# Kernel optimization log

Hardware: AMD Instinct MI355X
Metric: run time of the kernel (lower is better)

## Reference

```python
import jax, jax.numpy as jnp
import numpy as np

N, E = 50000, 1600000
IN_DIM, EMBED, OUT = 512, 128, 64


def setup_inputs() -> dict:
    key = jax.random.key(0)
    k = jax.random.split(key, 8)
    x = jax.random.normal(k[0], (N, IN_DIM), dtype=jnp.float32)
    edge_index = jax.random.randint(k[1], (2, E), 0, N, dtype=jnp.int32)
    W_dense = jax.random.normal(k[2], (EMBED, IN_DIM), dtype=jnp.float32) * 0.02
    b_dense = jnp.zeros((EMBED,), dtype=jnp.float32)
    W_gat = jax.random.normal(k[3], (OUT, EMBED), dtype=jnp.float32) * 0.05
    att_src = jax.random.normal(k[4], (OUT,), dtype=jnp.float32) * 0.1
    att_dst = jax.random.normal(k[5], (OUT,), dtype=jnp.float32) * 0.1
    b_gat = jnp.zeros((OUT,), dtype=jnp.float32)
    return {"x": x, "edge_index": edge_index, "W_dense": W_dense, "b_dense": b_dense,
            "W_gat": W_gat, "att_src": att_src, "att_dst": att_dst, "b_gat": b_gat}


def reference(x, edge_index, W_dense, b_dense, W_gat, att_src, att_dst, b_gat):
    # dense -> LeakyReLU(0.01) (nn.LeakyReLU default)
    h = jax.nn.leaky_relu(x @ W_dense.T + b_dense, negative_slope=0.01)  # [N, EMBED]
    n = h.shape[0]
    # GATConv (PyG, heads=1, add_self_loops=True, negative_slope=0.2)
    loops = jnp.arange(n, dtype=edge_index.dtype)
    src = jnp.concatenate([edge_index[0], loops])
    dst = jnp.concatenate([edge_index[1], loops])
    g = h @ W_gat.T  # [N, OUT]
    a_src = g @ att_src  # [N]
    a_dst = g @ att_dst  # [N]
    e = jax.nn.leaky_relu(a_src[src] + a_dst[dst], negative_slope=0.2)  # [E+N]
    # segment softmax over destination neighborhoods (self loops guarantee non-empty)
    m = jax.ops.segment_max(e, dst, num_segments=n)
    e = jnp.exp(e - m[dst])
    denom = jax.ops.segment_sum(e, dst, num_segments=n)
    alpha = e / denom[dst]
    out = jax.ops.segment_sum(g[src] * alpha[:, None], dst, num_segments=n) + b_gat
    # original returns ([embed_x], [embed_x]); we return the single embedding tensor
    return out
```

## Files before the change

### kernel.cpp

```cpp
#include <hip/hip_runtime.h>
#include <math.h>

#define IN_DIM 512
#define EMBED 128
#define OUT_DIM 64
#define NBPAD 256
#define SEGSH 12
#define CAP_LDS 10240

typedef __attribute__((ext_vector_type(8))) short bf16x8;
typedef __attribute__((ext_vector_type(4))) float f32x4;

__device__ __forceinline__ float lrelu(float v, float s) { return v > 0.f ? v : v * s; }

__device__ __forceinline__ float readlane_f(float v, int l) {
  return __int_as_float(__builtin_amdgcn_readlane(__float_as_int(v), l));
}

__device__ __forceinline__ unsigned short f2bf(float f) {
  unsigned int u = __float_as_uint(f);
  u += 0x7fff + ((u >> 16) & 1);
  return (unsigned short)(u >> 16);
}
__device__ __forceinline__ float bf2f(unsigned short h) {
  return __uint_as_float(((unsigned int)h) << 16);
}

__device__ __forceinline__ unsigned int cvt_pk_bf16(float a, float b) {
  unsigned int r;
  asm("v_cvt_pk_bf16_f32 %0, %1, %2" : "=v"(r) : "v"(a), "v"(b));
  return r;
}

__device__ __forceinline__ void gl_lds16(const void* g, void* l) {
  __builtin_amdgcn_global_load_lds(
      (const __attribute__((address_space(1))) unsigned int*)g,
      (__attribute__((address_space(3))) unsigned int*)l, 16, 0, 0);
}

#define LDA 40

__global__ __launch_bounds__(256) void split_w_kernel(
    const float* __restrict__ W, unsigned short* __restrict__ Wh,
    unsigned short* __restrict__ Wl, int total) {
  int i = (blockIdx.x * 256 + threadIdx.x) * 4;
  if (i >= total) return;
  float4 v = *(const float4*)(W + i);
  unsigned int h0 = cvt_pk_bf16(v.x, v.y);
  unsigned int h1 = cvt_pk_bf16(v.z, v.w);
  float r0 = v.x - __uint_as_float(h0 << 16);
  float r1 = v.y - __uint_as_float(h0 & 0xffff0000u);
  float r2 = v.z - __uint_as_float(h1 << 16);
  float r3 = v.w - __uint_as_float(h1 & 0xffff0000u);
  unsigned int l0 = cvt_pk_bf16(r0, r1);
  unsigned int l1 = cvt_pk_bf16(r2, r3);
  uint2 hh = make_uint2(h0, h1);
  uint2 ll = make_uint2(l0, l1);
  *(uint2*)(Wh + i) = hh;
  *(uint2*)(Wl + i) = ll;
}

__global__ __launch_bounds__(256) void gemm1_mfma_kernel(
    const float* __restrict__ x, const unsigned short* __restrict__ Wdh,
    const unsigned short* __restrict__ Wdl, const float* __restrict__ bd,
    float* __restrict__ h, int N) {
  __shared__ __align__(16) unsigned char Afp[16384];
  __shared__ __align__(16) unsigned char Bhs[8192];
  __shared__ __align__(16) unsigned char Bls[8192];

  const int tid = threadIdx.x;
  const int lane = tid & 63;
  const int wid = tid >> 6;
  const int mblk = blockIdx.x * 128;
  const int quad = lane >> 4;
  const int l15 = lane & 15;

  const char* asrc[4];
  void* adst[4];
#pragma unroll
  for (int i = 0; i < 4; ++i) {
    int chunk = i * 256 + tid;
    int row = chunk >> 3, ch = chunk & 7;
    int rg = mblk + row;
    if (rg >= N) rg = N - 1;
    asrc[i] = (const char*)x + (size_t)rg * (IN_DIM * 4) + ((ch ^ (row & 7)) << 4);
    adst[i] = Afp + chunk * 16;
  }
  const char* bsrcH[2];
  const char* bsrcL[2];
  void* bdstH[2];
  void* bdstL[2];
#pragma unroll
  for (int i = 0; i < 2; ++i) {
    int chunk = i * 256 + tid;
    int row = chunk >> 2, ch = chunk & 3;
    int cs = ch ^ ((row >> 1) & 3);
    size_t srcoff = (size_t)row * (IN_DIM * 2) + (cs << 4);
    bsrcH[i] = (const char*)Wdh + srcoff;
    bsrcL[i] = (const char*)Wdl + srcoff;
    bdstH[i] = Bhs + chunk * 16;
    bdstL[i] = Bls + chunk * 16;
  }

  f32x4 acc[2][8];
#pragma unroll
  for (int i = 0; i < 2; ++i)
#pragma unroll
    for (int j = 0; j < 8; ++j) acc[i][j] = (f32x4){0.f, 0.f, 0.f, 0.f};

  int aoff[2][2];
#pragma unroll
  for (int mi = 0; mi < 2; ++mi) {
    int row = wid * 32 + mi * 16 + l15;
    int sw = (row & 7) << 4;
#pragma unroll
    for (int hf = 0; hf < 2; ++hf)
      aoff[mi][hf] = row * 128 + (((quad << 5) | (hf << 4)) ^ sw);
  }
  int boff[8];
#pragma unroll
  for (int ni = 0; ni < 8; ++ni) {
    int row = ni * 16 + l15;
    boff[ni] = row * 64 + ((quad ^ ((row >> 1) & 3)) << 4);
  }

  for (int k0 = 0; k0 < IN_DIM; k0 += 32) {
    __syncthreads();
    const size_t ka = (size_t)k0 * 4;
    const size_t kb = (size_t)k0 * 2;
#pragma unroll
    for (int i = 0; i < 4; ++i) gl_lds16(asrc[i] + ka, adst[i]);
#pragma unroll
    for (int i = 0; i < 2; ++i) {
      gl_lds16(bsrcH[i] + kb, bdstH[i]);
      gl_lds16(bsrcL[i] + kb, bdstL[i]);
    }
    __syncthreads();

    bf16x8 AH[2], AL[2];
#pragma unroll
    for (int mi = 0; mi < 2; ++mi) {
      float4 f0 = *(const float4*)(Afp + aoff[mi][0]);
      float4 f1 = *(const float4*)(Afp + aoff[mi][1]);
      float av[8] = {f0.x, f0.y, f0.z, f0.w, f1.x, f1.y, f1.z, f1.w};
      union { unsigned int u[4]; bf16x8 v; } H, L;
#pragma unroll
      for (int i = 0; i < 4; ++i) {
        unsigned int hp = cvt_pk_bf16(av[2 * i], av[2 * i + 1]);
        float q0 = av[2 * i] - __uint_as_float(hp << 16);
        float q1 = av[2 * i + 1] - __uint_as_float(hp & 0xffff0000u);
        H.u[i] = hp;
        L.u[i] = cvt_pk_bf16(q0, q1);
      }
      AH[mi] = H.v;
      AL[mi] = L.v;
    }

#pragma unroll
    for (int hf = 0; hf < 2; ++hf) {
      bf16x8 BH[4], BL[4];
#pragma unroll
      for (int j = 0; j < 4; ++j) {
        BH[j] = *(const bf16x8*)(Bhs + boff[hf * 4 + j]);
        BL[j] = *(const bf16x8*)(Bls + boff[hf * 4 + j]);
      }
#pragma unroll
      for (int mi = 0; mi < 2; ++mi)
#pragma unroll
        for (int j = 0; j < 4; ++j) {
          int ni = hf * 4 + j;
          acc[mi][ni] = __builtin_amdgcn_mfma_f32_16x16x32_bf16(AH[mi], BH[j], acc[mi][ni], 0, 0, 0);
          acc[mi][ni] = __builtin_amdgcn_mfma_f32_16x16x32_bf16(AL[mi], BH[j], acc[mi][ni], 0, 0, 0);
          acc[mi][ni] = __builtin_amdgcn_mfma_f32_16x16x32_bf16(AH[mi], BL[j], acc[mi][ni], 0, 0, 0);
        }
    }
  }

#pragma unroll
  for (int mi = 0; mi < 2; ++mi)
#pragma unroll
    for (int ni = 0; ni < 8; ++ni) {
      int n = ni * 16 + l15;
      float b = bd[n];
#pragma unroll
      for (int r = 0; r < 4; ++r) {
        int m = mblk + wid * 32 + mi * 16 + quad * 4 + r;
        if (m < N) h[(size_t)m * EMBED + n] = lrelu(acc[mi][ni][r] + b, 0.01f);
      }
    }
}

__global__ __launch_bounds__(256) void gemm2_mfma_kernel(
    const float* __restrict__ h, const float* __restrict__ Wg,
    const float* __restrict__ att_src, const float* __restrict__ att_dst,
    float* __restrict__ g, float* __restrict__ a_src, float* __restrict__ a_dst,
    int N) {
  __shared__ __align__(16) unsigned short Ah[128][LDA];
  __shared__ __align__(16) unsigned short Al[128][LDA];
  __shared__ __align__(16) unsigned short Bh[64][LDA];
  __shared__ __align__(16) unsigned short Bl[64][LDA];

  const int tid = threadIdx.x;
  const int lane = tid & 63;
  const int wid = tid >> 6;
  const int wr = wid >> 1, wc = wid & 1;
  const int mblk = blockIdx.x * 128;
  const int quad = lane >> 4;
  const int l15 = lane & 15;

  const int arow = tid >> 1, acb = (tid & 1) * 16;
  const int brow = tid >> 2, bcb = (tid & 3) * 8;
  const bool avalid = (mblk + arow) < N;
  const float* aptr = h + (size_t)(mblk + arow) * EMBED + acb;
  const float* bptr = Wg + (size_t)brow * EMBED + bcb;

  f32x4 acc[4][2];
#pragma unroll
  for (int i = 0; i < 4; ++i)
#pragma unroll
    for (int j = 0; j < 2; ++j) acc[i][j] = (f32x4){0.f, 0.f, 0.f, 0.f};

  float4 t0, t1, t2, t3, u0, u1;
  auto do_load = [&](int k0) {
    if (avalid) {
      t0 = *(const float4*)(aptr + k0);
      t1 = *(const float4*)(aptr + k0 + 4);
      t2 = *(const float4*)(aptr + k0 + 8);
      t3 = *(const float4*)(aptr + k0 + 12);
    } else {
      t0 = t1 = t2 = t3 = make_float4(0.f, 0.f, 0.f, 0.f);
    }
    u0 = *(const float4*)(bptr + k0);
    u1 = *(const float4*)(bptr + k0 + 4);
  };
  do_load(0);

  for (int k0 = 0; k0 < EMBED; k0 += 32) {
    float av[16] = {t0.x, t0.y, t0.z, t0.w, t1.x, t1.y, t1.z, t1.w,
                    t2.x, t2.y, t2.z, t2.w, t3.x, t3.y, t3.z, t3.w};
    union { unsigned short us[16]; uint4 v[2]; } AH, AL;
#pragma unroll
    for (int i = 0; i < 16; ++i) {
      unsigned short hi = f2bf(av[i]);
      AH.us[i] = hi;
      AL.us[i] = f2bf(av[i] - bf2f(hi));
    }
    float bv[8] = {u0.x, u0.y, u0.z, u0.w, u1.x, u1.y, u1.z, u1.w};
    union { unsigned short us[8]; uint4 v; } BH, BL;
#pragma unroll
    for (int i = 0; i < 8; ++i) {
      unsigned short hi = f2bf(bv[i]);
      BH.us[i] = hi;
      BL.us[i] = f2bf(bv[i] - bf2f(hi));
    }

    __syncthreads();
    *(uint4*)&Ah[arow][acb] = AH.v[0];
    *(uint4*)&Ah[arow][acb + 8] = AH.v[1];
    *(uint4*)&Al[arow][acb] = AL.v[0];
    *(uint4*)&Al[arow][acb + 8] = AL.v[1];
    *(uint4*)&Bh[brow][bcb] = BH.v;
    *(uint4*)&Bl[brow][bcb] = BL.v;
    __syncthreads();

    if (k0 + 32 < EMBED) do_load(k0 + 32);

    bf16x8 ah[4], al[4], bh[2], bl[2];
#pragma unroll
    for (int mi = 0; mi < 4; ++mi) {
      int r = wr * 64 + mi * 16 + l15;
      ah[mi] = *(const bf16x8*)&Ah[r][quad * 8];
      al[mi] = *(const bf16x8*)&Al[r][quad * 8];
    }
#pragma unroll
    for (int ni = 0; ni < 2; ++ni) {
      int r = wc * 32 + ni * 16 + l15;
      bh[ni] = *(const bf16x8*)&Bh[r][quad * 8];
      bl[ni] = *(const bf16x8*)&Bl[r][quad * 8];
    }
#pragma unroll
    for (int mi = 0; mi < 4; ++mi)
#pragma unroll
      for (int ni = 0; ni < 2; ++ni) {
        acc[mi][ni] = __builtin_amdgcn_mfma_f32_16x16x32_bf16(ah[mi], bh[ni], acc[mi][ni], 0, 0, 0);
        acc[mi][ni] = __builtin_amdgcn_mfma_f32_16x16x32_bf16(al[mi], bh[ni], acc[mi][ni], 0, 0, 0);
        acc[mi][ni] = __builtin_amdgcn_mfma_f32_16x16x32_bf16(ah[mi], bl[ni], acc[mi][ni], 0, 0, 0);
      }
  }

  float as_[2], ad_[2];
#pragma unroll
  for (int ni = 0; ni < 2; ++ni) {
    int n = wc * 32 + ni * 16 + l15;
    as_[ni] = att_src[n];
    ad_[ni] = att_dst[n];
  }
#pragma unroll
  for (int mi = 0; mi < 4; ++mi) {
#pragma unroll
    for (int r = 0; r < 4; ++r) {
      int m = mblk + wr * 64 + mi * 16 + quad * 4 + r;
      float ps = acc[mi][0][r] * as_[0] + acc[mi][1][r] * as_[1];
      float pd = acc[mi][0][r] * ad_[0] + acc[mi][1][r] * ad_[1];
#pragma unroll
      for (int d = 1; d < 16; d <<= 1) {
        ps += __shfl_xor(ps, d, 64);
        pd += __shfl_xor(pd, d, 64);
      }
      if (m < N) {
#pragma unroll
        for (int ni = 0; ni < 2; ++ni) {
          int n = wc * 32 + ni * 16 + l15;
          g[(size_t)m * OUT_DIM + n] = acc[mi][ni][r];
        }
        if (l15 == 0 && wc == 0) {
          a_src[m] = ps;
          a_dst[m] = pd;
        }
      }
    }
  }
  __syncthreads();
#pragma unroll
  for (int mi = 0; mi < 4; ++mi) {
#pragma unroll
    for (int r = 0; r < 4; ++r) {
      int m = mblk + wr * 64 + mi * 16 + quad * 4 + r;
      float ps = acc[mi][0][r] * as_[0] + acc[mi][1][r] * as_[1];
      float pd = acc[mi][0][r] * ad_[0] + acc[mi][1][r] * ad_[1];
#pragma unroll
      for (int d = 1; d < 16; d <<= 1) {
        ps += __shfl_xor(ps, d, 64);
        pd += __shfl_xor(pd, d, 64);
      }
      if (m < N && l15 == 0 && wc == 1) {
        atomicAdd(&a_src[m], ps);
        atomicAdd(&a_dst[m], pd);
      }
    }
  }
}

__global__ __launch_bounds__(256) void hist_count_kernel(
    const int* __restrict__ ei, int* __restrict__ histT, int nblkP, int E,
    int N) {
  __shared__ int cnt[NBPAD];
  const int t = threadIdx.x;
  cnt[t] = 0;
  __syncthreads();
  const int T = E + N;
  const int base = blockIdx.x << SEGSH;
#pragma unroll
  for (int q = 0; q < (1 << SEGSH) / 256; ++q) {
    int i = base + q * 256 + t;
    if (i < T) {
      int d = (i < E) ? ei[E + i] : (i - E);
      atomicAdd(&cnt[d >> 8], 1);
    }
  }
  __syncthreads();
  histT[(size_t)t * nblkP + blockIdx.x] = cnt[t];
}

__global__ __launch_bounds__(256) void row_scan_kernel(
    int* __restrict__ histT, int* __restrict__ bucket_tot, int nblkP) {
  __shared__ int sc[256];
  const int t = threadIdx.x;
  int* row = histT + (size_t)blockIdx.x * nblkP;
  const int per = (nblkP + 255) / 256;
  int loc[8];
  int sum = 0;
#pragma unroll 4
  for (int j = 0; j < per; ++j) {
    int idx = t * per + j;
    int v = (idx < nblkP) ? row[idx] : 0;
    loc[j] = sum;
    sum += v;
  }
  sc[t] = sum;
  __syncthreads();
  for (int dlt = 1; dlt < 256; dlt <<= 1) {
    int add = (t >= dlt) ? sc[t - dlt] : 0;
    __syncthreads();
    sc[t] += add;
    __syncthreads();
  }
  const int off = sc[t] - sum;
#pragma unroll 4
  for (int j = 0; j < per; ++j) {
    int idx = t * per + j;
    if (idx < nblkP) row[idx] = off + loc[j];
  }
  if (t == 255) bucket_tot[blockIdx.x] = sc[255];
}

__global__ __launch_bounds__(256) void base_scan_kernel(
    const int* __restrict__ bucket_tot, int* __restrict__ bucket_base,
    int* __restrict__ offsets, int N, int T) {
  __shared__ int sc[256];
  const int t = threadIdx.x;
  int v = bucket_tot[t];
  sc[t] = v;
  __syncthreads();
  for (int dlt = 1; dlt < 256; dlt <<= 1) {
    int add = (t >= dlt) ? sc[t - dlt] : 0;
    __syncthreads();
    sc[t] += add;
    __syncthreads();
  }
  bucket_base[t] = sc[t] - v;
  if (t == 0) offsets[N] = T;
}

__global__ __launch_bounds__(256) void bin_kernel(
    const int* __restrict__ ei, const int* __restrict__ histT,
    const int* __restrict__ bucket_base, int* __restrict__ stageB, int nblkP,
    int E, int N) {
  __shared__ int cnt[NBPAD];
  __shared__ int basev[NBPAD];
  const int t = threadIdx.x;
  cnt[t] = 0;
  basev[t] = bucket_base[t] + histT[(size_t)t * nblkP + blockIdx.x];
  __syncthreads();
  const int T = E + N;
  const int base = blockIdx.x << SEGSH;
#pragma unroll
  for (int q = 0; q < (1 << SEGSH) / 256; ++q) {
    int i = base + q * 256 + t;
    if (i < T) {
      int s, d;
      if (i < E) {
        s = ei[i];
        d = ei[E + i];
      } else {
        s = d = i - E;
      }
      int b = d >> 8;
      int r = atomicAdd(&cnt[b], 1);
      stageB[basev[b] + r] = (s << 8) | (d & 255);
    }
  }
}

__global__ __launch_bounds__(256) void build_kernel(
    const int* __restrict__ stageB, const int* __restrict__ bucket_base,
    const int* __restrict__ bucket_tot, const float* __restrict__ a_src,
    const float* __restrict__ a_dst, int* __restrict__ offsets,
    int2* __restrict__ csr_pack, int N) {
  __shared__ int cnt[256];
  __shared__ int pre[256];
  __shared__ int cur[256];
  __shared__ int2 buf[CAP_LDS];
  const int b = blockIdx.x;
  const int t = threadIdx.x;
  const int base = bucket_base[b];
  const int tot = bucket_tot[b];
  cnt[t] = 0;
  __syncthreads();
  const int* sp = stageB + base;
  for (int i = t; i < tot; i += 256) atomicAdd(&cnt[sp[i] & 255], 1);
  __syncthreads();
  int v = cnt[t];
  pre[t] = v;
  __syncthreads();
  for (int dlt = 1; dlt < 256; dlt <<= 1) {
    int add = (t >= dlt) ? pre[t - dlt] : 0;
    __syncthreads();
    pre[t] += add;
    __syncthreads();
  }
  const int excl = pre[t] - v;
  cur[t] = excl;
  const int d_self = (b << 8) | t;
  if (d_self < N) offsets[d_self] = base + excl;
  __syncthreads();
  for (int i = t; i < tot; i += 256) {
    int rec = sp[i];
    int dl = rec & 255;
    int s = rec >> 8;
    float e = a_src[s] + a_dst[(b << 8) | dl];
    e = e > 0.f ? e : 0.2f * e;
    int pos = atomicAdd(&cur[dl], 1);
    int2 r2 = make_int2(s, __float_as_int(e));
    if (pos < CAP_LDS)
      buf[pos] = r2;
    else
      csr_pack[base + pos] = r2;
  }
  __syncthreads();
  const int lim = min(tot, CAP_LDS);
  for (int i = t; i < lim; i += 256) csr_pack[base + i] = buf[i];
}

__global__ __launch_bounds__(256) void aggregate_kernel(
    const int* __restrict__ offsets, const int2* __restrict__ csr_pack,
    const float* __restrict__ g, const float* __restrict__ b_gat,
    float* __restrict__ out, int N) {
  const int lane = threadIdx.x & 63;
  const int node = blockIdx.x * 4 + (threadIdx.x >> 6);
  if (node >= N) return;
  const int beg = offsets[node], end = offsets[node + 1];

  float m = -1e30f;
  for (int j = beg + lane; j < end; j += 64)
    m = fmaxf(m, __int_as_float(csr_pack[j].y));
#pragma unroll
  for (int d = 1; d < 64; d <<= 1) m = fmaxf(m, __shfl_xor(m, d, 64));

  float l = 0.f;
  for (int j = beg + lane; j < end; j += 64)
    l += __expf(__int_as_float(csr_pack[j].y) - m);
#pragma unroll
  for (int d = 1; d < 64; d <<= 1) l += __shfl_xor(l, d, 64);
  const float inv_l = 1.f / l;

  float acc0 = 0.f, acc1 = 0.f, acc2 = 0.f, acc3 = 0.f;
  for (int jb = beg; jb < end; jb += 64) {
    int j = jb + lane;
    float p = 0.f;
    int s = 0;
    if (j < end) {
      int2 rec = csr_pack[j];
      p = __expf(__int_as_float(rec.y) - m) * inv_l;
      s = rec.x;
    }
    const int cnt = min(64, end - jb);
    int jj = 0;
    for (; jj + 4 <= cnt; jj += 4) {
      int s0 = __builtin_amdgcn_readlane(s, jj);
      int s1 = __builtin_amdgcn_readlane(s, jj + 1);
      int s2 = __builtin_amdgcn_readlane(s, jj + 2);
      int s3 = __builtin_amdgcn_readlane(s, jj + 3);
      float p0 = readlane_f(p, jj);
      float p1 = readlane_f(p, jj + 1);
      float p2 = readlane_f(p, jj + 2);
      float p3 = readlane_f(p, jj + 3);
      acc0 += p0 * g[((size_t)s0 << 6) + lane];
      acc1 += p1 * g[((size_t)s1 << 6) + lane];
      acc2 += p2 * g[((size_t)s2 << 6) + lane];
      acc3 += p3 * g[((size_t)s3 << 6) + lane];
    }
    for (; jj < cnt; ++jj) {
      int s0 = __builtin_amdgcn_readlane(s, jj);
      float p0 = readlane_f(p, jj);
      acc0 += p0 * g[((size_t)s0 << 6) + lane];
    }
  }
  out[(size_t)node * OUT_DIM + lane] = (acc0 + acc1) + (acc2 + acc3) + b_gat[lane];
}

extern "C" void kernel_launch(void* const* d_in, const int* in_sizes, int n_in,
                              void* d_out, int out_size, void* d_ws, size_t ws_size,
                              hipStream_t stream) {
  const float* x = (const float*)d_in[0];
  const int* ei = (const int*)d_in[1];
  const float* Wd = (const float*)d_in[2];
  const float* bd = (const float*)d_in[3];
  const float* Wg = (const float*)d_in[4];
  const float* att_src = (const float*)d_in[5];
  const float* att_dst = (const float*)d_in[6];
  const float* bg = (const float*)d_in[7];
  float* out = (float*)d_out;

  const int N = in_sizes[0] / IN_DIM;
  const int E = in_sizes[1] / 2;
  const int T = E + N;
  const int NB = (N + 255) >> 8;
  const int nblkP = (T + (1 << SEGSH) - 1) >> SEGSH;

  char* ws = (char*)d_ws;
  size_t off = 0;
  auto alloc = [&](size_t bytes) -> void* {
    void* p = ws + off;
    off += (bytes + 15) & ~(size_t)15;
    return p;
  };
  float* h = (float*)alloc((size_t)N * EMBED * 4);
  float* g = (float*)alloc((size_t)N * OUT_DIM * 4);
  float* a_src = (float*)alloc((size_t)N * 4);
  float* a_dst = (float*)alloc((size_t)N * 4);
  int* offsets = (int*)alloc((size_t)(N + 1) * 4);
  int* histT = (int*)alloc((size_t)NBPAD * nblkP * 4);
  int* bucket_base = (int*)alloc((size_t)NBPAD * 4);
  int* bucket_tot = (int*)alloc((size_t)NBPAD * 4);
  int* stageB = (int*)alloc((size_t)T * 4);
  int2* csr_pack = (int2*)alloc((size_t)T * 8);
  unsigned short* Wdh = (unsigned short*)alloc((size_t)EMBED * IN_DIM * 2);
  unsigned short* Wdl = (unsigned short*)alloc((size_t)EMBED * IN_DIM * 2);

  const int WTOT = EMBED * IN_DIM;
  hipLaunchKernelGGL(split_w_kernel, dim3(WTOT / 1024), dim3(256), 0, stream,
                     Wd, Wdh, Wdl, WTOT);
  hipLaunchKernelGGL(gemm1_mfma_kernel, dim3((N + 127) / 128), dim3(256), 0,
                     stream, x, Wdh, Wdl, bd, h, N);
  hipLaunchKernelGGL(gemm2_mfma_kernel, dim3((N + 127) / 128), dim3(256), 0,
                     stream, h, Wg, att_src, att_dst, g, a_src, a_dst, N);
  hipLaunchKernelGGL(hist_count_kernel, dim3(nblkP), dim3(256), 0, stream,
                     ei, histT, nblkP, E, N);
  hipLaunchKernelGGL(row_scan_kernel, dim3(NBPAD), dim3(256), 0, stream,
                     histT, bucket_tot, nblkP);
  hipLaunchKernelGGL(base_scan_kernel, dim3(1), dim3(256), 0, stream,
                     bucket_tot, bucket_base, offsets, N, T);
  hipLaunchKernelGGL(bin_kernel, dim3(nblkP), dim3(256), 0, stream,
                     ei, histT, bucket_base, stageB, nblkP, E, N);
  hipLaunchKernelGGL(build_kernel, dim3(NB), dim3(256), 0, stream,
                     stageB, bucket_base, bucket_tot, a_src, a_dst, offsets,
                     csr_pack, N);
  hipLaunchKernelGGL(aggregate_kernel, dim3((N + 3) / 4), dim3(256), 0, stream,
                     offsets, csr_pack, g, bg, out, N);
}
```

Baseline: 315.9 us.

## Halve gemm1 row tile and process two nodes per wavefront in aggregation

The first GEMM now uses 64-row tiles instead of 128, which doubles the grid and cuts per-block LDS and accumulator registers to raise occupancy over the 50k-row problem. The aggregation kernel now splits each wavefront into two 32-lane halves, each handling one destination node and loading float2 feature pairs via shuffles instead of readlane. With about 33 edges per node on average, this avoids leaving half the lanes idle on the softmax and gather loops. The cost is less B-tile reuse in the GEMM and divergence when the two nodes in a wave have different degrees.

```diff
diff --git a/kernel.cpp b/kernel.cpp
--- a/kernel.cpp
+++ b/kernel.cpp
@@ -64,21 +64,21 @@
     const float* __restrict__ x, const unsigned short* __restrict__ Wdh,
     const unsigned short* __restrict__ Wdl, const float* __restrict__ bd,
     float* __restrict__ h, int N) {
-  __shared__ __align__(16) unsigned char Afp[16384];
+  __shared__ __align__(16) unsigned char Afp[8192];
   __shared__ __align__(16) unsigned char Bhs[8192];
   __shared__ __align__(16) unsigned char Bls[8192];
 
   const int tid = threadIdx.x;
   const int lane = tid & 63;
   const int wid = tid >> 6;
-  const int mblk = blockIdx.x * 128;
+  const int mblk = blockIdx.x * 64;
   const int quad = lane >> 4;
   const int l15 = lane & 15;
 
-  const char* asrc[4];
-  void* adst[4];
-#pragma unroll
-  for (int i = 0; i < 4; ++i) {
+  const char* asrc[2];
+  void* adst[2];
+#pragma unroll
+  for (int i = 0; i < 2; ++i) {
     int chunk = i * 256 + tid;
     int row = chunk >> 3, ch = chunk & 7;
     int rg = mblk + row;
@@ -102,20 +102,17 @@
     bdstL[i] = Bls + chunk * 16;
   }
 
-  f32x4 acc[2][8];
-#pragma unroll
-  for (int i = 0; i < 2; ++i)
-#pragma unroll
-    for (int j = 0; j < 8; ++j) acc[i][j] = (f32x4){0.f, 0.f, 0.f, 0.f};
-
-  int aoff[2][2];
-#pragma unroll
-  for (int mi = 0; mi < 2; ++mi) {
-    int row = wid * 32 + mi * 16 + l15;
+  f32x4 acc[8];
+#pragma unroll
+  for (int j = 0; j < 8; ++j) acc[j] = (f32x4){0.f, 0.f, 0.f, 0.f};
+
+  int aoff[2];
+  {
+    int row = wid * 16 + l15;
     int sw = (row & 7) << 4;
 #pragma unroll
     for (int hf = 0; hf < 2; ++hf)
-      aoff[mi][hf] = row * 128 + (((quad << 5) | (hf << 4)) ^ sw);
+      aoff[hf] = row * 128 + (((quad << 5) | (hf << 4)) ^ sw);
   }
   int boff[8];
 #pragma unroll
@@ -129,7 +126,7 @@
     const size_t ka = (size_t)k0 * 4;
     const size_t kb = (size_t)k0 * 2;
 #pragma unroll
-    for (int i = 0; i < 4; ++i) gl_lds16(asrc[i] + ka, adst[i]);
+    for (int i = 0; i < 2; ++i) gl_lds16(asrc[i] + ka, adst[i]);
 #pragma unroll
     for (int i = 0; i < 2; ++i) {
       gl_lds16(bsrcH[i] + kb, bdstH[i]);
@@ -137,11 +134,10 @@
     }
     __syncthreads();
 
-    bf16x8 AH[2], AL[2];
-#pragma unroll
-    for (int mi = 0; mi < 2; ++mi) {
-      float4 f0 = *(const float4*)(Afp + aoff[mi][0]);
-      float4 f1 = *(const float4*)(Afp + aoff[mi][1]);
+    bf16x8 AH, AL;
+    {
+      float4 f0 = *(const float4*)(Afp + aoff[0]);
+      float4 f1 = *(const float4*)(Afp + aoff[1]);
       float av[8] = {f0.x, f0.y, f0.z, f0.w, f1.x, f1.y, f1.z, f1.w};
       union { unsigned int u[4]; bf16x8 v; } H, L;
 #pragma unroll
@@ -152,8 +148,8 @@
         H.u[i] = hp;
         L.u[i] = cvt_pk_bf16(q0, q1);
       }
-      AH[mi] = H.v;
-      AL[mi] = L.v;
+      AH = H.v;
+      AL = L.v;
     }
 
 #pragma unroll
@@ -165,29 +161,25 @@
         BL[j] = *(const bf16x8*)(Bls + boff[hf * 4 + j]);
       }
 #pragma unroll
-      for (int mi = 0; mi < 2; ++mi)
-#pragma unroll
-        for (int j = 0; j < 4; ++j) {
-          int ni = hf * 4 + j;
-          acc[mi][ni] = __builtin_amdgcn_mfma_f32_16x16x32_bf16(AH[mi], BH[j], acc[mi][ni], 0, 0, 0);
-          acc[mi][ni] = __builtin_amdgcn_mfma_f32_16x16x32_bf16(AL[mi], BH[j], acc[mi][ni], 0, 0, 0);
-          acc[mi][ni] = __builtin_amdgcn_mfma_f32_16x16x32_bf16(AH[mi], BL[j], acc[mi][ni], 0, 0, 0);
-        }
-    }
-  }
-
-#pragma unroll
-  for (int mi = 0; mi < 2; ++mi)
-#pragma unroll
-    for (int ni = 0; ni < 8; ++ni) {
-      int n = ni * 16 + l15;
-      float b = bd[n];
-#pragma unroll
-      for (int r = 0; r < 4; ++r) {
-        int m = mblk + wid * 32 + mi * 16 + quad * 4 + r;
-        if (m < N) h[(size_t)m * EMBED + n] = lrelu(acc[mi][ni][r] + b, 0.01f);
-      }
-    }
+      for (int j = 0; j < 4; ++j) {
+        int ni = hf * 4 + j;
+        acc[ni] = __builtin_amdgcn_mfma_f32_16x16x32_bf16(AH, BH[j], acc[ni], 0, 0, 0);
+        acc[ni] = __builtin_amdgcn_mfma_f32_16x16x32_bf16(AL, BH[j], acc[ni], 0, 0, 0);
+        acc[ni] = __builtin_amdgcn_mfma_f32_16x16x32_bf16(AH, BL[j], acc[ni], 0, 0, 0);
+      }
+    }
+  }
+
+#pragma unroll
+  for (int ni = 0; ni < 8; ++ni) {
+    int n = ni * 16 + l15;
+    float b = bd[n];
+#pragma unroll
+    for (int r = 0; r < 4; ++r) {
+      int m = mblk + wid * 16 + quad * 4 + r;
+      if (m < N) h[(size_t)m * EMBED + n] = lrelu(acc[ni][r] + b, 0.01f);
+    }
+  }
 }
 
 __global__ __launch_bounds__(256) void gemm2_mfma_kernel(
@@ -497,26 +489,34 @@
     const float* __restrict__ g, const float* __restrict__ b_gat,
     float* __restrict__ out, int N) {
   const int lane = threadIdx.x & 63;
-  const int node = blockIdx.x * 4 + (threadIdx.x >> 6);
-  if (node >= N) return;
-  const int beg = offsets[node], end = offsets[node + 1];
+  const int half = lane >> 5;
+  const int hl = lane & 31;
+  const int node = blockIdx.x * 8 + (threadIdx.x >> 6) * 2 + half;
+  const bool valid = node < N;
+  const int beg = valid ? offsets[node] : 0;
+  const int end = valid ? offsets[node + 1] : 0;
 
   float m = -1e30f;
-  for (int j = beg + lane; j < end; j += 64)
+  for (int j = beg + hl; j < end; j += 32)
     m = fmaxf(m, __int_as_float(csr_pack[j].y));
 #pragma unroll
-  for (int d = 1; d < 64; d <<= 1) m = fmaxf(m, __shfl_xor(m, d, 64));
+  for (int d = 1; d < 32; d <<= 1) m = fmaxf(m, __shfl_xor(m, d, 64));
 
   float l = 0.f;
-  for (int j = beg + lane; j < end; j += 64)
+  for (int j = beg + hl; j < end; j += 32)
     l += __expf(__int_as_float(csr_pack[j].y) - m);
 #pragma unroll
-  for (int d = 1; d < 64; d <<= 1) l += __shfl_xor(l, d, 64);
+  for (int d = 1; d < 32; d <<= 1) l += __shfl_xor(l, d, 64);
   const float inv_l = 1.f / l;
 
-  float acc0 = 0.f, acc1 = 0.f, acc2 = 0.f, acc3 = 0.f;
-  for (int jb = beg; jb < end; jb += 64) {
-    int j = jb + lane;
+  int iters = (end - beg + 31) >> 5;
+  iters = max(iters, __shfl_xor(iters, 32, 64));
+
+  const float* gp = g + hl * 2;
+  const int sb = half << 5;
+  float ax0 = 0.f, ay0 = 0.f, ax1 = 0.f, ay1 = 0.f;
+  for (int it = 0; it < iters; ++it) {
+    int j = beg + it * 32 + hl;
     float p = 0.f;
     int s = 0;
     if (j < end) {
@@ -524,29 +524,36 @@
       p = __expf(__int_as_float(rec.y) - m) * inv_l;
       s = rec.x;
     }
-    const int cnt = min(64, end - jb);
+    int cnt = end - beg - it * 32;
+    cnt = max(0, min(32, cnt));
+    int mc = max(cnt, __shfl_xor(cnt, 32, 64));
     int jj = 0;
-    for (; jj + 4 <= cnt; jj += 4) {
-      int s0 = __builtin_amdgcn_readlane(s, jj);
-      int s1 = __builtin_amdgcn_readlane(s, jj + 1);
-      int s2 = __builtin_amdgcn_readlane(s, jj + 2);
-      int s3 = __builtin_amdgcn_readlane(s, jj + 3);
-      float p0 = readlane_f(p, jj);
-      float p1 = readlane_f(p, jj + 1);
-      float p2 = readlane_f(p, jj + 2);
-      float p3 = readlane_f(p, jj + 3);
-      acc0 += p0 * g[((size_t)s0 << 6) + lane];
-      acc1 += p1 * g[((size_t)s1 << 6) + lane];
-      acc2 += p2 * g[((size_t)s2 << 6) + lane];
-      acc3 += p3 * g[((size_t)s3 << 6) + lane];
-    }
-    for (; jj < cnt; ++jj) {
-      int s0 = __builtin_amdgcn_readlane(s, jj);
-      float p0 = readlane_f(p, jj);
-      acc0 += p0 * g[((size_t)s0 << 6) + lane];
-    }
-  }
-  out[(size_t)node * OUT_DIM + lane] = (acc0 + acc1) + (acc2 + acc3) + b_gat[lane];
+    for (; jj + 2 <= mc; jj += 2) {
+      int s0 = __shfl(s, sb + jj, 64);
+      int s1 = __shfl(s, sb + jj + 1, 64);
+      float p0 = __shfl(p, sb + jj, 64);
+      float p1 = __shfl(p, sb + jj + 1, 64);
+      float2 g0 = *(const float2*)(gp + ((size_t)s0 << 6));
+      float2 g1 = *(const float2*)(gp + ((size_t)s1 << 6));
+      ax0 += p0 * g0.x;
+      ay0 += p0 * g0.y;
+      ax1 += p1 * g1.x;
+      ay1 += p1 * g1.y;
+    }
+    for (; jj < mc; ++jj) {
+      int s0 = __shfl(s, sb + jj, 64);
+      float p0 = __shfl(p, sb + jj, 64);
+      float2 g0 = *(const float2*)(gp + ((size_t)s0 << 6));
+      ax0 += p0 * g0.x;
+      ay0 += p0 * g0.y;
+    }
+  }
+  if (valid) {
+    float2 o;
+    o.x = ax0 + ax1 + b_gat[hl * 2];
+    o.y = ay0 + ay1 + b_gat[hl * 2 + 1];
+    *(float2*)(out + (size_t)node * OUT_DIM + hl * 2) = o;
+  }
 }
 
 extern "C" void kernel_launch(void* const* d_in, const int* in_sizes, int n_in,
@@ -591,7 +598,7 @@
   const int WTOT = EMBED * IN_DIM;
   hipLaunchKernelGGL(split_w_kernel, dim3(WTOT / 1024), dim3(256), 0, stream,
                      Wd, Wdh, Wdl, WTOT);
-  hipLaunchKernelGGL(gemm1_mfma_kernel, dim3((N + 127) / 128), dim3(256), 0,
+  hipLaunchKernelGGL(gemm1_mfma_kernel, dim3((N + 63) / 64), dim3(256), 0,
                      stream, x, Wdh, Wdl, bd, h, N);
   hipLaunchKernelGGL(gemm2_mfma_kernel, dim3((N + 127) / 128), dim3(256), 0,
                      stream, h, Wg, att_src, att_dst, g, a_src, a_dst, N);
@@ -606,6 +613,6 @@
   hipLaunchKernelGGL(build_kernel, dim3(NB), dim3(256), 0, stream,
                      stageB, bucket_base, bucket_tot, a_src, a_dst, offsets,
                      csr_pack, N);
-  hipLaunchKernelGGL(aggregate_kernel, dim3((N + 3) / 4), dim3(256), 0, stream,
+  hipLaunchKernelGGL(aggregate_kernel, dim3((N + 7) / 8), dim3(256), 0, stream,
                      offsets, csr_pack, g, bg, out, N);
 }
```

After: 335.1 us. +6.1%, slower.

## Double-buffer weight tiles and load x directly to registers in dense GEMM

Applied to the files above, without the earlier changes.

The first GEMM kernel no longer stages x tiles through LDS. Each lane reads its own fp32 A fragment straight from global memory into registers and prefetches the next k-step while the current one is converted and multiplied. The bf16 hi/lo weight tiles are double-buffered in LDS, so the next tile's global-to-LDS copy overlaps the current MFMA work, and the loop needs one barrier per step instead of two. The cost is extra registers for the prefetched A data. The direct x reads are also only 32-byte chunks per lane rather than cooperative coalesced loads, which may hurt global memory efficiency.

```diff
diff --git a/kernel.cpp b/kernel.cpp
--- a/kernel.cpp
+++ b/kernel.cpp
@@ -64,9 +64,8 @@
     const float* __restrict__ x, const unsigned short* __restrict__ Wdh,
     const unsigned short* __restrict__ Wdl, const float* __restrict__ bd,
     float* __restrict__ h, int N) {
-  __shared__ __align__(16) unsigned char Afp[16384];
-  __shared__ __align__(16) unsigned char Bhs[8192];
-  __shared__ __align__(16) unsigned char Bls[8192];
+  __shared__ __align__(16) unsigned char Bhs[2][8192];
+  __shared__ __align__(16) unsigned char Bls[2][8192];
 
   const int tid = threadIdx.x;
   const int lane = tid & 63;
@@ -75,21 +74,25 @@
   const int quad = lane >> 4;
   const int l15 = lane & 15;
 
-  const char* asrc[4];
-  void* adst[4];
-#pragma unroll
-  for (int i = 0; i < 4; ++i) {
-    int chunk = i * 256 + tid;
-    int row = chunk >> 3, ch = chunk & 7;
-    int rg = mblk + row;
+  const float* aptr[2];
+#pragma unroll
+  for (int mi = 0; mi < 2; ++mi) {
+    int rg = mblk + wid * 32 + mi * 16 + l15;
     if (rg >= N) rg = N - 1;
-    asrc[i] = (const char*)x + (size_t)rg * (IN_DIM * 4) + ((ch ^ (row & 7)) << 4);
-    adst[i] = Afp + chunk * 16;
-  }
+    aptr[mi] = x + (size_t)rg * IN_DIM + quad * 8;
+  }
+  float4 tc[2][2];
+  auto loadA = [&](int k0) {
+#pragma unroll
+    for (int mi = 0; mi < 2; ++mi) {
+      tc[mi][0] = *(const float4*)(aptr[mi] + k0);
+      tc[mi][1] = *(const float4*)(aptr[mi] + k0 + 4);
+    }
+  };
+
   const char* bsrcH[2];
   const char* bsrcL[2];
-  void* bdstH[2];
-  void* bdstL[2];
+  int bdst[2];
 #pragma unroll
   for (int i = 0; i < 2; ++i) {
     int chunk = i * 256 + tid;
@@ -98,25 +101,17 @@
     size_t srcoff = (size_t)row * (IN_DIM * 2) + (cs << 4);
     bsrcH[i] = (const char*)Wdh + srcoff;
     bsrcL[i] = (const char*)Wdl + srcoff;
-    bdstH[i] = Bhs + chunk * 16;
-    bdstL[i] = Bls + chunk * 16;
-  }
-
-  f32x4 acc[2][8];
-#pragma unroll
-  for (int i = 0; i < 2; ++i)
-#pragma unroll
-    for (int j = 0; j < 8; ++j) acc[i][j] = (f32x4){0.f, 0.f, 0.f, 0.f};
-
-  int aoff[2][2];
-#pragma unroll
-  for (int mi = 0; mi < 2; ++mi) {
-    int row = wid * 32 + mi * 16 + l15;
-    int sw = (row & 7) << 4;
-#pragma unroll
-    for (int hf = 0; hf < 2; ++hf)
-      aoff[mi][hf] = row * 128 + (((quad << 5) | (hf << 4)) ^ sw);
-  }
+    bdst[i] = chunk * 16;
+  }
+  auto stageB = [&](int buf, int k0) {
+    const size_t kb = (size_t)k0 * 2;
+#pragma unroll
+    for (int i = 0; i < 2; ++i) {
+      gl_lds16(bsrcH[i] + kb, Bhs[buf] + bdst[i]);
+      gl_lds16(bsrcL[i] + kb, Bls[buf] + bdst[i]);
+    }
+  };
+
   int boff[8];
 #pragma unroll
   for (int ni = 0; ni < 8; ++ni) {
@@ -124,25 +119,26 @@
     boff[ni] = row * 64 + ((quad ^ ((row >> 1) & 3)) << 4);
   }
 
-  for (int k0 = 0; k0 < IN_DIM; k0 += 32) {
-    __syncthreads();
-    const size_t ka = (size_t)k0 * 4;
-    const size_t kb = (size_t)k0 * 2;
-#pragma unroll
-    for (int i = 0; i < 4; ++i) gl_lds16(asrc[i] + ka, adst[i]);
-#pragma unroll
-    for (int i = 0; i < 2; ++i) {
-      gl_lds16(bsrcH[i] + kb, bdstH[i]);
-      gl_lds16(bsrcL[i] + kb, bdstL[i]);
-    }
-    __syncthreads();
+  f32x4 acc[2][8];
+#pragma unroll
+  for (int i = 0; i < 2; ++i)
+#pragma unroll
+    for (int j = 0; j < 8; ++j) acc[i][j] = (f32x4){0.f, 0.f, 0.f, 0.f};
+
+  stageB(0, 0);
+  loadA(0);
+  __syncthreads();
+
+#pragma unroll 2
+  for (int s = 0; s < IN_DIM / 32; ++s) {
+    const int buf = s & 1;
+    if (s + 1 < IN_DIM / 32) stageB(buf ^ 1, (s + 1) * 32);
 
     bf16x8 AH[2], AL[2];
 #pragma unroll
     for (int mi = 0; mi < 2; ++mi) {
-      float4 f0 = *(const float4*)(Afp + aoff[mi][0]);
-      float4 f1 = *(const float4*)(Afp + aoff[mi][1]);
-      float av[8] = {f0.x, f0.y, f0.z, f0.w, f1.x, f1.y, f1.z, f1.w};
+      float av[8] = {tc[mi][0].x, tc[mi][0].y, tc[mi][0].z, tc[mi][0].w,
+                     tc[mi][1].x, tc[mi][1].y, tc[mi][1].z, tc[mi][1].w};
       union { unsigned int u[4]; bf16x8 v; } H, L;
 #pragma unroll
       for (int i = 0; i < 4; ++i) {
@@ -155,14 +151,15 @@
       AH[mi] = H.v;
       AL[mi] = L.v;
     }
+    if (s + 1 < IN_DIM / 32) loadA((s + 1) * 32);
 
 #pragma unroll
     for (int hf = 0; hf < 2; ++hf) {
       bf16x8 BH[4], BL[4];
 #pragma unroll
       for (int j = 0; j < 4; ++j) {
-        BH[j] = *(const bf16x8*)(Bhs + boff[hf * 4 + j]);
-        BL[j] = *(const bf16x8*)(Bls + boff[hf * 4 + j]);
+        BH[j] = *(const bf16x8*)(Bhs[buf] + boff[hf * 4 + j]);
+        BL[j] = *(const bf16x8*)(Bls[buf] + boff[hf * 4 + j]);
       }
 #pragma unroll
       for (int mi = 0; mi < 2; ++mi)
@@ -174,6 +171,7 @@
           acc[mi][ni] = __builtin_amdgcn_mfma_f32_16x16x32_bf16(AH[mi], BL[j], acc[mi][ni], 0, 0, 0);
         }
     }
+    __syncthreads();
   }
 
 #pragma unroll
```

After: 322.6 us. +2.1%, slower.
